# Kernel tuning notes

Hardware: AMD Instinct MI355X
Metric: run time of the kernel (lower is better)

Reference implementation:

```python
import jax, jax.numpy as jnp
import numpy as np
import math

B, S, E, H, DFF = 8, 1024, 1024, 16, 4096
DK = E // H
EPS = 1e-6


def _layernorm(x, alpha, bias):
    # Faithful to the torch module: uses unbiased std (ddof=1) and divides by (std + eps)
    mean = jnp.mean(x, axis=-1, keepdims=True)
    var = jnp.sum((x - mean) ** 2, axis=-1, keepdims=True) / (x.shape[-1] - 1)
    std = jnp.sqrt(var)
    return alpha * (x - mean) / (std + EPS) + bias


def setup_inputs() -> dict:
    key = jax.random.key(0)
    ks = jax.random.split(key, 16)
    sc_e = 1.0 / math.sqrt(E)
    sc_f = 1.0 / math.sqrt(DFF)
    inp = {
        "x": jax.random.normal(ks[0], (B, S, E), dtype=jnp.float32),
        "mask": jnp.ones((1, 1, S, S), dtype=jnp.int32),
        # linear weights stored as (in, out)
        "wq": jax.random.normal(ks[1], (E, E), jnp.float32) * sc_e,
        "bq": jnp.zeros((E,), jnp.float32),
        "wk": jax.random.normal(ks[2], (E, E), jnp.float32) * sc_e,
        "bk": jnp.zeros((E,), jnp.float32),
        "wv": jax.random.normal(ks[3], (E, E), jnp.float32) * sc_e,
        "bv": jnp.zeros((E,), jnp.float32),
        "wo": jax.random.normal(ks[4], (E, E), jnp.float32) * sc_e,
        "bo": jnp.zeros((E,), jnp.float32),
        "w1": jax.random.normal(ks[5], (E, DFF), jnp.float32) * sc_e,
        "b1": jnp.zeros((DFF,), jnp.float32),
        "w2": jax.random.normal(ks[6], (DFF, E), jnp.float32) * sc_f,
        "b2": jnp.zeros((E,), jnp.float32),
        "ln1_a": jnp.ones((E,), jnp.float32),
        "ln1_b": jnp.zeros((E,), jnp.float32),
        "ln2_a": jnp.ones((E,), jnp.float32),
        "ln2_b": jnp.zeros((E,), jnp.float32),
    }
    return inp


def _mha(x, mask, wq, bq, wk, bk, wv, bv, wo, bo):
    q = (x @ wq + bq).reshape(B, S, H, DK).transpose(0, 2, 1, 3)  # [B,H,S,DK]
    k = (x @ wk + bk).reshape(B, S, H, DK).transpose(0, 2, 1, 3)
    v = (x @ wv + bv).reshape(B, S, H, DK).transpose(0, 2, 1, 3)
    scores = jnp.einsum("bhqd,bhkd->bhqk", q, k) / math.sqrt(DK)  # [B,H,S,S]
    scores = jnp.where(mask == 0, jnp.float32(-1e9), scores)
    attn = jax.nn.softmax(scores, axis=-1)
    out = jnp.einsum("bhqk,bhkd->bhqd", attn, v)  # [B,H,S,DK]
    out = out.transpose(0, 2, 1, 3).reshape(B, S, E)
    return out @ wo + bo


def reference(x, mask, wq, bq, wk, bk, wv, bv, wo, bo, w1, b1, w2, b2,
              ln1_a, ln1_b, ln2_a, ln2_b):
    # Residual connection 1 (pre-norm): x + dropout(attn(norm(x))) ; dropout=0 at eval
    h1 = x + _mha(_layernorm(x, ln1_a, ln1_b), mask, wq, bq, wk, bk, wv, bv, wo, bo)
    # Residual connection 2: h1 + ffn(norm(h1))
    n2 = _layernorm(h1, ln2_a, ln2_b)
    ff = jax.nn.relu(n2 @ w1 + b1) @ w2 + b2
    return h1 + ff
```

## Files before the change

kernel.cpp:

```cpp
#include <hip/hip_runtime.h>
#include <hip/hip_bf16.h>
#include <cstdint>
#include <cstddef>

#define BB   8
#define SS   1024
#define EE   1024
#define HH   16
#define DKK  64
#define DFFN 4096
#define NROWS (BB*SS)

#define QSCALE 0.18033688011112042f

typedef __attribute__((ext_vector_type(8))) short short8;
typedef __attribute__((ext_vector_type(4))) short s16x4;
typedef __attribute__((ext_vector_type(4))) float f32x4;

__device__ __forceinline__ short f2bf(float f) {
  __hip_bfloat16 h = __float2bfloat16(f);
  return __builtin_bit_cast(short, h);
}

__device__ __forceinline__ float fexp2(float x) {
  float r;
  asm("v_exp_f32 %0, %1" : "=v"(r) : "v"(x));
  return r;
}

__device__ __forceinline__ void gload_lds16(const void* g, void* l) {
  __builtin_amdgcn_global_load_lds((const __attribute__((address_space(1))) void*)g,
                                   (__attribute__((address_space(3))) void*)l, 16, 0, 0);
}

__device__ __forceinline__ f32x4 mfma16(s16x4 a, s16x4 b, f32x4 c) {
#if __has_builtin(__builtin_amdgcn_mfma_f32_16x16x16_bf16)
  return __builtin_amdgcn_mfma_f32_16x16x16_bf16(a, b, c, 0, 0, 0);
#elif __has_builtin(__builtin_amdgcn_mfma_f32_16x16x16bf16_1k)
  return __builtin_amdgcn_mfma_f32_16x16x16bf16_1k(a, b, c, 0, 0, 0);
#else
  f32x4 d = c;
  asm("v_mfma_f32_16x16x16_bf16 %0, %1, %2, %0" : "+v"(d) : "v"(a), "v"(b));
  return d;
#endif
}

__global__ __launch_bounds__(256) void prep_kernel(
    const float* __restrict__ wq, const float* __restrict__ wk,
    const float* __restrict__ wv, const float* __restrict__ wo,
    const float* __restrict__ w1, const float* __restrict__ w2,
    const float* __restrict__ bq, const float* __restrict__ bk,
    const float* __restrict__ bv,
    short* __restrict__ wqkvT, short* __restrict__ woT,
    short* __restrict__ w1T, short* __restrict__ w2T,
    float* __restrict__ bqkv) {
  int bid = blockIdx.x;
  int tx = threadIdx.x, ty = threadIdx.y;
  if (bid >= 12288) {
    int t = ty * 32 + tx;
    for (int i = t; i < EE; i += 256) {
      bqkv[i] = bq[i];
      bqkv[EE + i] = bk[i];
      bqkv[2 * EE + i] = bv[i];
    }
    return;
  }
  const float* in;
  short* out;
  int R, C, t;
  if (bid < 1024)      { in = wq; out = wqkvT;                 R = EE;   C = EE;   t = bid; }
  else if (bid < 2048) { in = wk; out = wqkvT + 1024 * 1024;   R = EE;   C = EE;   t = bid - 1024; }
  else if (bid < 3072) { in = wv; out = wqkvT + 2 * 1024 * 1024; R = EE; C = EE;   t = bid - 2048; }
  else if (bid < 4096) { in = wo; out = woT;                   R = EE;   C = EE;   t = bid - 3072; }
  else if (bid < 8192) { in = w1; out = w1T;                   R = EE;   C = DFFN; t = bid - 4096; }
  else                 { in = w2; out = w2T;                   R = DFFN; C = EE;   t = bid - 8192; }
  int ntx = C >> 5;
  int c0 = (t % ntx) * 32, r0 = (t / ntx) * 32;
  __shared__ float tile[32][33];
#pragma unroll
  for (int i = 0; i < 32; i += 8)
    tile[ty + i][tx] = in[(size_t)(r0 + ty + i) * C + (c0 + tx)];
  __syncthreads();
#pragma unroll
  for (int i = 0; i < 32; i += 8)
    out[(size_t)(c0 + ty + i) * R + (r0 + tx)] = f2bf(tile[tx][ty + i]);
}

__global__ __launch_bounds__(256) void ln_kernel(const float* __restrict__ x,
                                                 const float* __restrict__ alpha,
                                                 const float* __restrict__ beta,
                                                 short* __restrict__ out) {
  __shared__ float sbuf[4];
  int row = blockIdx.x;
  int tid = threadIdx.x;
  const float* xr = x + (size_t)row * EE;
  float4 v = reinterpret_cast<const float4*>(xr)[tid];
  float s = v.x + v.y + v.z + v.w;
#pragma unroll
  for (int o = 32; o > 0; o >>= 1) s += __shfl_down(s, o);
  if ((tid & 63) == 0) sbuf[tid >> 6] = s;
  __syncthreads();
  float mean = (sbuf[0] + sbuf[1] + sbuf[2] + sbuf[3]) * (1.0f / EE);
  __syncthreads();
  float dx = v.x - mean, dy = v.y - mean, dz = v.z - mean, dw = v.w - mean;
  float sq = dx * dx + dy * dy + dz * dz + dw * dw;
#pragma unroll
  for (int o = 32; o > 0; o >>= 1) sq += __shfl_down(sq, o);
  if ((tid & 63) == 0) sbuf[tid >> 6] = sq;
  __syncthreads();
  float var = (sbuf[0] + sbuf[1] + sbuf[2] + sbuf[3]) * (1.0f / (EE - 1));
  float inv = 1.0f / (sqrtf(var) + 1e-6f);
  float4 a = reinterpret_cast<const float4*>(alpha)[tid];
  float4 b = reinterpret_cast<const float4*>(beta)[tid];
  size_t base = (size_t)row * EE + tid * 4;
  out[base + 0] = f2bf(a.x * dx * inv + b.x);
  out[base + 1] = f2bf(a.y * dy * inv + b.y);
  out[base + 2] = f2bf(a.z * dz * inv + b.z);
  out[base + 3] = f2bf(a.w * dw * inv + b.w);
}

template <int EPI>
__global__ __launch_bounds__(512, 2) void gemm256(const short* __restrict__ A,
                                                  const short* __restrict__ Bt,
                                                  const float* __restrict__ bias,
                                                  const float* __restrict__ resid,
                                                  void* __restrict__ out,
                                                  int N, int K, int NTN) {
  extern __shared__ char lds[];
  int tid = threadIdx.x, lane = tid & 63, w = tid >> 6;
  int wm = w >> 2, wn = w & 3;
  int g = lane >> 4, c = lane & 15;

  int nwg = gridDim.x, wg = blockIdx.x;
  int swg = (wg & 7) * (nwg >> 3) + (wg >> 3);
  int mt = swg / NTN, nt = swg % NTN;
  int m0 = mt * 256, n0 = nt * 256;

  int rS = tid >> 3;
  int gslot = (tid & 7) ^ ((tid >> 4) & 7);
  const short* pA = A + (size_t)(m0 + rS) * K + gslot * 8;
  const short* pB = Bt + (size_t)(n0 + rS) * K + gslot * 8;

#define STAGE_A(b, h, T)                                                                   \
  {                                                                                        \
    gload_lds16(pA + (size_t)((h)*128) * K + (size_t)(T)*64,                               \
                lds + (b)*32768 + (h)*16384 + tid * 16);                                   \
    gload_lds16(pA + (size_t)((h)*128 + 64) * K + (size_t)(T)*64,                          \
                lds + (b)*32768 + (h)*16384 + 8192 + tid * 16);                            \
  }
#define STAGE_B(b, h, T)                                                                   \
  {                                                                                        \
    gload_lds16(pB + (size_t)((h)*128) * K + (size_t)(T)*64,                               \
                lds + 65536 + (b)*32768 + (h)*16384 + tid * 16);                           \
    gload_lds16(pB + (size_t)((h)*128 + 64) * K + (size_t)(T)*64,                          \
                lds + 65536 + (b)*32768 + (h)*16384 + 8192 + tid * 16);                    \
  }
#define WAITV(NN) asm volatile("s_waitcnt vmcnt(" #NN ")" ::: "memory")

  int aoff0 = ((0 * 4 + g) ^ (c >> 1)) * 16;
  int aoff1 = ((1 * 4 + g) ^ (c >> 1)) * 16;
  char* ldsAb = lds + (wm * 128 + c) * 128;
  char* ldsBb = lds + 65536 + (wn * 64 + c) * 128;

  f32x4 acc[8][4] = {};
  short8 af[2][2], bfr[4][2];

#define READB(b)                                                                           \
  {                                                                                        \
    _Pragma("unroll") for (int nf = 0; nf < 4; ++nf) {                                     \
      bfr[nf][0] = *(const short8*)(ldsBb + (b)*32768 + nf * 2048 + aoff0);                \
      bfr[nf][1] = *(const short8*)(ldsBb + (b)*32768 + nf * 2048 + aoff1);                \
    }                                                                                      \
  }

#define PHASE(b, q, STAGEOP, ENDWAIT)                                                      \
  {                                                                                        \
    _Pragma("unroll") for (int mi = 0; mi < 2; ++mi) {                                     \
      af[mi][0] = *(const short8*)(ldsAb + (b)*32768 + ((q)*32 + mi * 16) * 128 + aoff0);  \
      af[mi][1] = *(const short8*)(ldsAb + (b)*32768 + ((q)*32 + mi * 16) * 128 + aoff1);  \
    }                                                                                      \
    STAGEOP;                                                                               \
    __builtin_amdgcn_s_barrier();                                                          \
    asm volatile("s_waitcnt lgkmcnt(0)" ::: "memory");                                     \
    __builtin_amdgcn_sched_barrier(0);                                                     \
    __builtin_amdgcn_s_setprio(1);                                                         \
    _Pragma("unroll") for (int mi = 0; mi < 2; ++mi)                                       \
      _Pragma("unroll") for (int nf = 0; nf < 4; ++nf) {                                   \
        acc[(q)*2 + mi][nf] = __builtin_amdgcn_mfma_f32_16x16x32_bf16(                     \
            af[mi][0], bfr[nf][0], acc[(q)*2 + mi][nf], 0, 0, 0);                          \
        acc[(q)*2 + mi][nf] = __builtin_amdgcn_mfma_f32_16x16x32_bf16(                     \
            af[mi][1], bfr[nf][1], acc[(q)*2 + mi][nf], 0, 0, 0);                          \
      }                                                                                    \
    __builtin_amdgcn_s_setprio(0);                                                         \
    ENDWAIT;                                                                               \
    __builtin_amdgcn_s_barrier();                                                          \
  }

  int NKT = K >> 6;

  STAGE_A(0, 0, 0); STAGE_A(0, 1, 0);
  STAGE_B(0, 0, 0); STAGE_B(0, 1, 0);
  STAGE_B(1, 0, 1); STAGE_B(1, 1, 1);
  WAITV(4);
  __builtin_amdgcn_s_barrier();

  for (int t = 0; t < NKT - 2; t += 2) {
    READB(0);
    PHASE(0, 0, STAGE_A(1, 0, t + 1), );
    PHASE(0, 1, STAGE_A(1, 1, t + 1), );
    PHASE(0, 2, STAGE_B(0, 0, t + 2), );
    PHASE(0, 3, STAGE_B(0, 1, t + 2), WAITV(4));
    READB(1);
    PHASE(1, 0, STAGE_A(0, 0, t + 2), );
    PHASE(1, 1, STAGE_A(0, 1, t + 2), );
    PHASE(1, 2, STAGE_B(1, 0, t + 3), );
    PHASE(1, 3, STAGE_B(1, 1, t + 3), WAITV(4));
  }
  {
    int t = NKT - 2;
    READB(0);
    PHASE(0, 0, STAGE_A(1, 0, t + 1), );
    PHASE(0, 1, STAGE_A(1, 1, t + 1), );
    PHASE(0, 2, , );
    PHASE(0, 3, , WAITV(0));
    READB(1);
    PHASE(1, 0, , );
    PHASE(1, 1, , );
    PHASE(1, 2, , );
    PHASE(1, 3, , );
  }

#undef STAGE_A
#undef STAGE_B
#undef READB
#undef PHASE
#undef WAITV

  int rb_ = m0 + wm * 128;
  int cb_ = n0 + wn * 64;
#pragma unroll
  for (int fm = 0; fm < 8; ++fm) {
#pragma unroll
    for (int nf = 0; nf < 4; ++nf) {
      int col = cb_ + nf * 16 + c;
      float bv = bias[col];
#pragma unroll
      for (int j = 0; j < 4; ++j) {
        int row = rb_ + fm * 16 + g * 4 + j;
        float val = acc[fm][nf][j] + bv;
        if (EPI == 1) {
          ((short*)out)[(size_t)row * N + col] = f2bf(val > 0.f ? val : 0.f);
        } else {
          ((float*)out)[(size_t)row * N + col] = resid[(size_t)row * N + col] + val;
        }
      }
    }
  }
}

template <int EPI>
__global__ __launch_bounds__(512, 1) void gemm256x128(const short* __restrict__ A,
                                                      const short* __restrict__ Bt,
                                                      const float* __restrict__ bias,
                                                      const float* __restrict__ resid,
                                                      void* __restrict__ out,
                                                      int N, int K, int NTN) {
  extern __shared__ char lds[];
  int tid = threadIdx.x, lane = tid & 63, w = tid >> 6;
  int wm = w >> 1, wn = w & 1;
  int g = lane >> 4, c = lane & 15;

  int nwg = gridDim.x, wg = blockIdx.x;
  int swg = (wg & 7) * (nwg >> 3) + (wg >> 3);
  int mt = swg / NTN, nt = swg % NTN;
  int m0 = mt * 256, n0 = nt * 128;

  int rS = tid >> 3;
  int gslot = (tid & 7) ^ ((tid >> 4) & 7);
  const short* pA = A + (size_t)(m0 + rS) * K + gslot * 8;
  const short* pB = Bt + (size_t)(n0 + rS) * K + gslot * 8;

#define STAGE_A(b, h, T)                                                                   \
  {                                                                                        \
    gload_lds16(pA + (size_t)((h)*128) * K + (size_t)(T)*64,                               \
                lds + (b)*32768 + (h)*16384 + tid * 16);                                   \
    gload_lds16(pA + (size_t)((h)*128 + 64) * K + (size_t)(T)*64,                          \
                lds + (b)*32768 + (h)*16384 + 8192 + tid * 16);                            \
  }
#define STAGE_B(b, T)                                                                      \
  {                                                                                        \
    gload_lds16(pB + (size_t)(T)*64,            lds + 65536 + (b)*16384 + tid * 16);       \
    gload_lds16(pB + (size_t)64 * K + (size_t)(T)*64,                                      \
                lds + 65536 + (b)*16384 + 8192 + tid * 16);                                \
  }
#define WAITV(NN) asm volatile("s_waitcnt vmcnt(" #NN ")" ::: "memory")

  int aoff0 = ((0 * 4 + g) ^ (c >> 1)) * 16;
  int aoff1 = ((1 * 4 + g) ^ (c >> 1)) * 16;
  char* ldsAb = lds + (wm * 64 + c) * 128;
  char* ldsBb = lds + 65536 + (wn * 64 + c) * 128;

  f32x4 acc[4][4] = {};
  short8 af[2][2], bfr[4][2];

#define READB(b)                                                                           \
  {                                                                                        \
    _Pragma("unroll") for (int nf = 0; nf < 4; ++nf) {                                     \
      bfr[nf][0] = *(const short8*)(ldsBb + (b)*16384 + nf * 2048 + aoff0);                \
      bfr[nf][1] = *(const short8*)(ldsBb + (b)*16384 + nf * 2048 + aoff1);                \
    }                                                                                      \
  }

#define PHASE(b, q, STAGEOP, ENDWAIT)                                                      \
  {                                                                                        \
    _Pragma("unroll") for (int mi = 0; mi < 2; ++mi) {                                     \
      af[mi][0] = *(const short8*)(ldsAb + (b)*32768 + ((q)*32 + mi * 16) * 128 + aoff0);  \
      af[mi][1] = *(const short8*)(ldsAb + (b)*32768 + ((q)*32 + mi * 16) * 128 + aoff1);  \
    }                                                                                      \
    STAGEOP;                                                                               \
    __builtin_amdgcn_s_barrier();                                                          \
    asm volatile("s_waitcnt lgkmcnt(0)" ::: "memory");                                     \
    __builtin_amdgcn_sched_barrier(0);                                                     \
    __builtin_amdgcn_s_setprio(1);                                                         \
    _Pragma("unroll") for (int mi = 0; mi < 2; ++mi)                                       \
      _Pragma("unroll") for (int nf = 0; nf < 4; ++nf) {                                   \
        acc[(q)*2 + mi][nf] = __builtin_amdgcn_mfma_f32_16x16x32_bf16(                     \
            af[mi][0], bfr[nf][0], acc[(q)*2 + mi][nf], 0, 0, 0);                          \
        acc[(q)*2 + mi][nf] = __builtin_amdgcn_mfma_f32_16x16x32_bf16(                     \
            af[mi][1], bfr[nf][1], acc[(q)*2 + mi][nf], 0, 0, 0);                          \
      }                                                                                    \
    __builtin_amdgcn_s_setprio(0);                                                         \
    ENDWAIT;                                                                               \
    __builtin_amdgcn_s_barrier();                                                          \
  }

  int NKT = K >> 6;

  STAGE_A(0, 0, 0); STAGE_A(0, 1, 0);
  STAGE_B(0, 0);
  STAGE_B(1, 1);
  WAITV(2);
  __builtin_amdgcn_s_barrier();

  for (int t = 0; t < NKT - 2; t += 2) {
    READB(0);
    PHASE(0, 0, STAGE_A(1, 0, t + 1); STAGE_A(1, 1, t + 1), );
    PHASE(0, 1, STAGE_B(0, t + 2), WAITV(2));
    READB(1);
    PHASE(1, 0, STAGE_A(0, 0, t + 2); STAGE_A(0, 1, t + 2), );
    PHASE(1, 1, STAGE_B(1, t + 3), WAITV(2));
  }
  READB(0);
  PHASE(0, 0, STAGE_A(1, 0, NKT - 1); STAGE_A(1, 1, NKT - 1), );
  PHASE(0, 1, , WAITV(0));
  READB(1);
  PHASE(1, 0, , );
  PHASE(1, 1, , );

#undef STAGE_A
#undef STAGE_B
#undef READB
#undef PHASE
#undef WAITV

  int rb_ = m0 + wm * 64;
  int cb_ = n0 + wn * 64;
#pragma unroll
  for (int fm = 0; fm < 4; ++fm) {
#pragma unroll
    for (int nf = 0; nf < 4; ++nf) {
      int col = cb_ + nf * 16 + c;
      float bv = bias[col];
      if (EPI == 5) {
        int which = col >> 10;
        int inner = col & 1023;
        int h = inner >> 6, d = inner & 63;
        if (which < 2) {
          short* dst = (short*)out + (size_t)which * (8u * 1024 * 1024);
#pragma unroll
          for (int j = 0; j < 4; ++j) {
            int row = rb_ + fm * 16 + g * 4 + j;
            int b = row >> 10, s = row & 1023;
            float val = acc[fm][nf][j] + bv;
            if (which == 0) val *= QSCALE;
            dst[(((size_t)(b * HH + h)) * SS + s) * DKK + d] = f2bf(val);
          }
        } else {
          int row0 = rb_ + fm * 16 + g * 4;
          int b = row0 >> 10, s0 = row0 & 1023;
          s16x4 pkv;
#pragma unroll
          for (int j = 0; j < 4; ++j) pkv[j] = f2bf(acc[fm][nf][j] + bv);
          *(s16x4*)((short*)out + 2u * 8 * 1024 * 1024 +
                    (((size_t)(b * HH + h)) * DKK + d) * SS + s0) = pkv;
        }
      } else {
#pragma unroll
        for (int j = 0; j < 4; ++j) {
          int row = rb_ + fm * 16 + g * 4 + j;
          ((float*)out)[(size_t)row * N + col] =
              resid[(size_t)row * N + col] + acc[fm][nf][j] + bv;
        }
      }
    }
  }
}

__global__ __launch_bounds__(256, 3) void attn_kernel(const short* __restrict__ q,
                                                      const short* __restrict__ k,
                                                      const short* __restrict__ vt,
                                                      short* __restrict__ out) {
  __shared__ short Ks[2][64 * 64];
  __shared__ short Vs[2][64 * 64];
  int bh = blockIdx.x, qt = blockIdx.y;
  int tid = threadIdx.x, lane = tid & 63, w = tid >> 6;
  int g = lane >> 4, c = lane & 15;
  const short* qp = q + (size_t)bh * SS * DKK;
  const short* kp = k + (size_t)bh * SS * DKK;
  const short* vp = vt + (size_t)bh * DKK * SS;

  int q0 = qt * 128 + w * 32;

  short8 qf[2][2];
#pragma unroll
  for (int qb = 0; qb < 2; ++qb)
#pragma unroll
    for (int ks = 0; ks < 2; ++ks)
      qf[qb][ks] = *(const short8*)(qp + (size_t)(q0 + qb * 16 + c) * DKK + ks * 32 + g * 8);

  f32x4 oacc[2][4];
#pragma unroll
  for (int qb = 0; qb < 2; ++qb)
#pragma unroll
    for (int nd = 0; nd < 4; ++nd)
#pragma unroll
      for (int j = 0; j < 4; ++j) oacc[qb][nd][j] = 0.f;
  float mrun[2] = {-1e30f, -1e30f}, lrun[2] = {0.f, 0.f};

  int rs = lane >> 3;
  int cs = lane & 7;
  int swz = (cs ^ rs) * 8;

  int buf = 0;
#define STAGE(B, T)                                                                  \
  {                                                                                  \
    _Pragma("unroll")                                                                \
    for (int cc = 0; cc < 2; ++cc) {                                                 \
      int chunk = w * 2 + cc;                                                        \
      int row = chunk * 8 + rs;                                                      \
      gload_lds16(kp + (size_t)((T) * 64 + row) * DKK + swz, &Ks[B][chunk * 512]);   \
      gload_lds16(vp + (size_t)row * SS + (T) * 64 + swz, &Vs[B][chunk * 512]);      \
    }                                                                                \
  }

  STAGE(0, 0);
  __syncthreads();

  for (int t = 0; t < SS / 64; ++t) {
    if (t < SS / 64 - 1) STAGE(buf ^ 1, t + 1);

    f32x4 sc[2][4];
#pragma unroll
    for (int qb = 0; qb < 2; ++qb)
#pragma unroll
      for (int nf = 0; nf < 4; ++nf)
#pragma unroll
        for (int j = 0; j < 4; ++j) sc[qb][nf][j] = 0.f;
    __builtin_amdgcn_s_setprio(1);
#pragma unroll
    for (int ks = 0; ks < 2; ++ks) {
      short8 kf[4];
#pragma unroll
      for (int nf = 0; nf < 4; ++nf) {
        int row = nf * 16 + c;
        int off = row * 64 + (((ks * 64 + g * 16) ^ ((c & 7) << 4)) >> 1);
        kf[nf] = *(const short8*)&Ks[buf][off];
      }
#pragma unroll
      for (int qb = 0; qb < 2; ++qb)
#pragma unroll
        for (int nf = 0; nf < 4; ++nf)
          sc[qb][nf] = __builtin_amdgcn_mfma_f32_16x16x32_bf16(kf[nf], qf[qb][ks], sc[qb][nf], 0, 0, 0);
    }
    __builtin_amdgcn_s_setprio(0);

    s16x4 pk[2][4];
#pragma unroll
    for (int qb = 0; qb < 2; ++qb) {
      float pm = -1e30f;
#pragma unroll
      for (int nf = 0; nf < 4; ++nf)
#pragma unroll
        for (int j = 0; j < 4; ++j) pm = fmaxf(pm, sc[qb][nf][j]);
      pm = fmaxf(pm, __shfl_xor(pm, 16));
      pm = fmaxf(pm, __shfl_xor(pm, 32));
      float mcur = mrun[qb];
      bool defer = __all(pm <= mcur + 8.0f);
      float mnew = defer ? mcur : fmaxf(mcur, pm);
      float rsum = 0.f;
#pragma unroll
      for (int nf = 0; nf < 4; ++nf) {
        float p0 = fexp2(sc[qb][nf][0] - mnew);
        float p1 = fexp2(sc[qb][nf][1] - mnew);
        float p2 = fexp2(sc[qb][nf][2] - mnew);
        float p3 = fexp2(sc[qb][nf][3] - mnew);
        rsum += (p0 + p1) + (p2 + p3);
        pk[qb][nf][0] = f2bf(p0); pk[qb][nf][1] = f2bf(p1);
        pk[qb][nf][2] = f2bf(p2); pk[qb][nf][3] = f2bf(p3);
      }
      rsum += __shfl_xor(rsum, 16);
      rsum += __shfl_xor(rsum, 32);
      if (defer) {
        lrun[qb] += rsum;
      } else {
        float corr = fexp2(mcur - mnew);
        mrun[qb] = mnew;
        lrun[qb] = lrun[qb] * corr + rsum;
        float cj[4];
#pragma unroll
        for (int j = 0; j < 4; ++j) cj[j] = __shfl(corr, (lane & 48) | (g * 4 + j));
#pragma unroll
        for (int nd = 0; nd < 4; ++nd)
#pragma unroll
          for (int j = 0; j < 4; ++j) oacc[qb][nd][j] *= cj[j];
      }
    }

    __builtin_amdgcn_s_setprio(1);
#pragma unroll
    for (int nf = 0; nf < 4; ++nf) {
      s16x4 vf[4];
#pragma unroll
      for (int nd = 0; nd < 4; ++nd) {
        int row = nd * 16 + c;
        int off = row * 64 + (((nf * 32 + g * 8) ^ ((c & 7) << 4)) >> 1);
        vf[nd] = *(const s16x4*)&Vs[buf][off];
      }
#pragma unroll
      for (int qb = 0; qb < 2; ++qb)
#pragma unroll
        for (int nd = 0; nd < 4; ++nd)
          oacc[qb][nd] = mfma16(pk[qb][nf], vf[nd], oacc[qb][nd]);
    }
    __builtin_amdgcn_s_setprio(0);
    __syncthreads();
    buf ^= 1;
  }
#undef STAGE

  int b = bh >> 4, h = bh & 15;
#pragma unroll
  for (int qb = 0; qb < 2; ++qb) {
#pragma unroll
    for (int j = 0; j < 4; ++j) {
      float linv = 1.0f / __shfl(lrun[qb], (lane & 48) | (g * 4 + j));
      int srow = q0 + qb * 16 + g * 4 + j;
#pragma unroll
      for (int nd = 0; nd < 4; ++nd)
        out[((size_t)b * SS + srow) * EE + h * DKK + nd * 16 + c] = f2bf(oacc[qb][nd][j] * linv);
    }
  }
}

extern "C" void kernel_launch(void* const* d_in, const int* in_sizes, int n_in,
                              void* d_out, int out_size, void* d_ws, size_t ws_size,
                              hipStream_t stream) {
  (void)in_sizes; (void)n_in; (void)out_size; (void)ws_size;
  const float* x   = (const float*)d_in[0];
  const float* wq  = (const float*)d_in[2];  const float* bq  = (const float*)d_in[3];
  const float* wk  = (const float*)d_in[4];  const float* bk  = (const float*)d_in[5];
  const float* wv  = (const float*)d_in[6];  const float* bv  = (const float*)d_in[7];
  const float* wo  = (const float*)d_in[8];  const float* bo  = (const float*)d_in[9];
  const float* w1  = (const float*)d_in[10]; const float* b1  = (const float*)d_in[11];
  const float* w2  = (const float*)d_in[12]; const float* b2  = (const float*)d_in[13];
  const float* l1a = (const float*)d_in[14]; const float* l1b = (const float*)d_in[15];
  const float* l2a = (const float*)d_in[16]; const float* l2b = (const float*)d_in[17];
  float* out = (float*)d_out;

  char* ws = (char*)d_ws;
  const size_t MB = 1024ull * 1024ull;
  short* wqkvT = (short*)(ws + 0 * MB);
  short* woT = (short*)(ws + 6 * MB);
  short* w1T = (short*)(ws + 8 * MB);
  short* w2T = (short*)(ws + 16 * MB);
  short* n1  = (short*)(ws + 24 * MB);
  short* qb  = (short*)(ws + 40 * MB);
  short* ff1 = (short*)(ws + 40 * MB);
  short* ao  = (short*)(ws + 88 * MB);
  float* bqkv = (float*)(ws + 100 * MB);
  float* h1  = (float*)(ws + 104 * MB);

  dim3 tb(32, 8);
  prep_kernel<<<dim3(12289), tb, 0, stream>>>(wq, wk, wv, wo, w1, w2, bq, bk, bv,
                                              wqkvT, woT, w1T, w2T, bqkv);

  ln_kernel<<<NROWS, 256, 0, stream>>>(x, l1a, l1b, n1);

  gemm256x128<5><<<dim3(32 * 24), 512, 98304, stream>>>(n1, wqkvT, bqkv, nullptr, qb, 3072, EE, 24);

  attn_kernel<<<dim3(BB * HH, SS / 128), 256, 0, stream>>>(qb, qb + 8 * 1024 * 1024,
                                                           qb + 16 * 1024 * 1024, ao);

  gemm256x128<2><<<dim3(256), 512, 98304, stream>>>(ao, woT, bo, x, h1, EE, EE, 8);

  ln_kernel<<<NROWS, 256, 0, stream>>>(h1, l2a, l2b, n1);

  gemm256<1><<<dim3(32 * 16), 512, 131072, stream>>>(n1, w1T, b1, nullptr, ff1, DFFN, EE, 16);
  gemm256x128<2><<<dim3(256), 512, 98304, stream>>>(ff1, w2T, b2, h1, out, EE, DFFN, 8);
}
```

Before: 354.6 us.

## Load K/V fragments directly from global memory in attention, drop LDS staging

```diff
diff --git a/kernel.cpp b/kernel.cpp
--- a/kernel.cpp
+++ b/kernel.cpp
@@ -406,13 +406,13 @@
   }
 }
 
-__global__ __launch_bounds__(256, 3) void attn_kernel(const short* __restrict__ q,
+__global__ __launch_bounds__(256, 4) void attn_kernel(const short* __restrict__ q,
                                                       const short* __restrict__ k,
                                                       const short* __restrict__ vt,
                                                       short* __restrict__ out) {
-  __shared__ short Ks[2][64 * 64];
-  __shared__ short Vs[2][64 * 64];
-  int bh = blockIdx.x, qt = blockIdx.y;
+  int x = blockIdx.x;
+  int bh = (x & 7) + 8 * (x >> 6);
+  int qt = (x >> 3) & 7;
   int tid = threadIdx.x, lane = tid & 63, w = tid >> 6;
   int g = lane >> 4, c = lane & 15;
   const short* qp = q + (size_t)bh * SS * DKK;
@@ -437,28 +437,10 @@
       for (int j = 0; j < 4; ++j) oacc[qb][nd][j] = 0.f;
   float mrun[2] = {-1e30f, -1e30f}, lrun[2] = {0.f, 0.f};
 
-  int rs = lane >> 3;
-  int cs = lane & 7;
-  int swz = (cs ^ rs) * 8;
-
-  int buf = 0;
-#define STAGE(B, T)                                                                  \
-  {                                                                                  \
-    _Pragma("unroll")                                                                \
-    for (int cc = 0; cc < 2; ++cc) {                                                 \
-      int chunk = w * 2 + cc;                                                        \
-      int row = chunk * 8 + rs;                                                      \
-      gload_lds16(kp + (size_t)((T) * 64 + row) * DKK + swz, &Ks[B][chunk * 512]);   \
-      gload_lds16(vp + (size_t)row * SS + (T) * 64 + swz, &Vs[B][chunk * 512]);      \
-    }                                                                                \
-  }
-
-  STAGE(0, 0);
-  __syncthreads();
+  const short* kbase = kp + (size_t)c * DKK + g * 8;
+  const short* vbase = vp + (size_t)c * SS + g * 4;
 
   for (int t = 0; t < SS / 64; ++t) {
-    if (t < SS / 64 - 1) STAGE(buf ^ 1, t + 1);
-
     f32x4 sc[2][4];
 #pragma unroll
     for (int qb = 0; qb < 2; ++qb)
@@ -471,11 +453,8 @@
     for (int ks = 0; ks < 2; ++ks) {
       short8 kf[4];
 #pragma unroll
-      for (int nf = 0; nf < 4; ++nf) {
-        int row = nf * 16 + c;
-        int off = row * 64 + (((ks * 64 + g * 16) ^ ((c & 7) << 4)) >> 1);
-        kf[nf] = *(const short8*)&Ks[buf][off];
-      }
+      for (int nf = 0; nf < 4; ++nf)
+        kf[nf] = *(const short8*)(kbase + (size_t)(t * 64 + nf * 16) * DKK + ks * 32);
 #pragma unroll
       for (int qb = 0; qb < 2; ++qb)
 #pragma unroll
@@ -531,11 +510,8 @@
     for (int nf = 0; nf < 4; ++nf) {
       s16x4 vf[4];
 #pragma unroll
-      for (int nd = 0; nd < 4; ++nd) {
-        int row = nd * 16 + c;
-        int off = row * 64 + (((nf * 32 + g * 8) ^ ((c & 7) << 4)) >> 1);
-        vf[nd] = *(const s16x4*)&Vs[buf][off];
-      }
+      for (int nd = 0; nd < 4; ++nd)
+        vf[nd] = *(const s16x4*)(vbase + (size_t)(nd * 16) * SS + t * 64 + nf * 16);
 #pragma unroll
       for (int qb = 0; qb < 2; ++qb)
 #pragma unroll
@@ -543,10 +519,7 @@
           oacc[qb][nd] = mfma16(pk[qb][nf], vf[nd], oacc[qb][nd]);
     }
     __builtin_amdgcn_s_setprio(0);
-    __syncthreads();
-    buf ^= 1;
-  }
-#undef STAGE
+  }
 
   int b = bh >> 4, h = bh & 15;
 #pragma unroll
@@ -598,8 +571,8 @@
 
   gemm256x128<5><<<dim3(32 * 24), 512, 98304, stream>>>(n1, wqkvT, bqkv, nullptr, qb, 3072, EE, 24);
 
-  attn_kernel<<<dim3(BB * HH, SS / 128), 256, 0, stream>>>(qb, qb + 8 * 1024 * 1024,
-                                                           qb + 16 * 1024 * 1024, ao);
+  attn_kernel<<<dim3(BB * HH * (SS / 128)), 256, 0, stream>>>(qb, qb + 8 * 1024 * 1024,
+                                                              qb + 16 * 1024 * 1024, ao);
 
   gemm256x128<2><<<dim3(256), 512, 98304, stream>>>(ao, woT, bo, x, h1, EE, EE, 8);
 
```

New measurement: 465.2 us. 1.31x slower.
